# Kernel tuning notes

Measured on AMD Instinct MI355X. Metric: run time of the kernel, lower is better.

## Reference

```python
import jax, jax.numpy as jnp
import numpy as np

B, N, D, H = 4, 8192, 1024, 16
HD = D // H  # head dim 64
EPS = 1e-5


def setup_inputs() -> dict:
    key = jax.random.key(0)
    ks = jax.random.split(key, 12)
    s = 1.0 / np.sqrt(D)
    return {
        "query": jax.random.normal(ks[0], (B, N, D), jnp.float32),
        "Wq": jax.random.normal(ks[1], (D, D), jnp.float32) * s,
        "bq": jax.random.normal(ks[2], (D,), jnp.float32) * 0.01,
        "Wk": jax.random.normal(ks[3], (D, D), jnp.float32) * s,
        "bk": jax.random.normal(ks[4], (D,), jnp.float32) * 0.01,
        "Wv": jax.random.normal(ks[5], (D, D), jnp.float32) * s,
        "bv": jax.random.normal(ks[6], (D,), jnp.float32) * 0.01,
        "Wu": jax.random.normal(ks[7], (D, D), jnp.float32) * s,
        "bu": jax.random.normal(ks[8], (D,), jnp.float32) * 0.01,
        "Wo": jax.random.normal(ks[9], (D, D), jnp.float32) * s,
        "bo": jax.random.normal(ks[10], (D,), jnp.float32) * 0.01,
        "ln_w": jnp.ones((D,), jnp.float32),
        "ln_b": jnp.zeros((D,), jnp.float32),
    }


def _abs_clamp(t, min_mag=0.01, max_mag=100.0):
    return jnp.clip(jnp.abs(t), min_mag, max_mag) * jnp.sign(t)


def _heads(x):  # [b, n, h*d] -> [b, h, n, d]
    b, n, _ = x.shape
    return x.reshape(b, n, H, HD).transpose(0, 2, 1, 3)


def reference(query, Wq, bq, Wk, bk, Wv, bv, Wu, bu, Wo, bo, ln_w, ln_b):
    q = jax.nn.relu(_heads(query @ Wq + bq))  # [b,h,n,d]
    k = jax.nn.relu(_heads(query @ Wk + bk))
    v = _heads(query @ Wv + bv)
    u = query @ Wu + bu  # [b,n,D]
    # global linear-attention reduction: kv[b,h,d,e] = sum_n k v
    kv = jnp.einsum('bhnd,bhne->bhde', k, v)
    kv = _abs_clamp(kv)
    out = jnp.einsum('bhnd,bhde->bhne', q, kv)  # [b,h,n,d]
    out = out.transpose(0, 2, 1, 3).reshape(query.shape)  # [b,n,D]
    # LayerNorm over last dim
    mu = jnp.mean(out, axis=-1, keepdims=True)
    var = jnp.var(out, axis=-1, keepdims=True)
    out = (out - mu) * jax.lax.rsqrt(var + EPS) * ln_w + ln_b
    out = u * out
    return out @ Wo + bo
```

## Files before the change

### kernel.cpp

```cpp
#include <hip/hip_runtime.h>

#define M_TOT 32768

typedef float f32x4 __attribute__((ext_vector_type(4)));
typedef short s16x8 __attribute__((ext_vector_type(8)));

#define AS1(p) ((__attribute__((address_space(1))) void*)(p))
#define AS3(p) ((__attribute__((address_space(3))) void*)(p))

#define BARRIER() asm volatile("s_barrier" ::: "memory")
#define VMCNT8() asm volatile("s_waitcnt vmcnt(8)" ::: "memory")
#define VMCNT4() asm volatile("s_waitcnt vmcnt(4)" ::: "memory")
#define VMCNT0() asm volatile("s_waitcnt vmcnt(0)" ::: "memory")

__device__ __forceinline__ short f2bf(float f) {
    unsigned u = __builtin_bit_cast(unsigned, f);
    u += 0x7fffu + ((u >> 16) & 1u);
    return (short)(u >> 16);
}
__device__ __forceinline__ float bf2f(short s) {
    unsigned u = ((unsigned)(unsigned short)s) << 16;
    return __builtin_bit_cast(float, u);
}

__global__ void conv_x(const float* __restrict__ x, short* __restrict__ y) {
    const size_t nchunk = (size_t)M_TOT * 1024 / 8;
    const size_t stride = (size_t)gridDim.x * blockDim.x;
    for (size_t c = (size_t)blockIdx.x * blockDim.x + threadIdx.x; c < nchunk; c += stride) {
        const float4* src = (const float4*)(x + c * 8);
        float4 a = src[0], b = src[1];
        s16x8 r;
        r[0] = f2bf(a.x); r[1] = f2bf(a.y); r[2] = f2bf(a.z); r[3] = f2bf(a.w);
        r[4] = f2bf(b.x); r[5] = f2bf(b.y); r[6] = f2bf(b.z); r[7] = f2bf(b.w);
        *(s16x8*)(y + c * 8) = r;
    }
}

__global__ void conv_w(const float* __restrict__ Wq, const float* __restrict__ Wk,
                       const float* __restrict__ Wv, const float* __restrict__ Wu,
                       const float* __restrict__ Wo, short* __restrict__ Wcat) {
    const int c = blockIdx.x * 256 + threadIdx.x;
    const int np = c >> 8;
    const int k0 = (c & 255) << 2;
    const float* W = (np < 1024) ? Wq : (np < 2048) ? Wk : (np < 3072) ? Wv
                   : (np < 4096) ? Wu : Wo;
    const int n = np & 1023;
    short4 r;
    r.x = f2bf(W[(size_t)(k0 + 0) * 1024 + n]);
    r.y = f2bf(W[(size_t)(k0 + 1) * 1024 + n]);
    r.z = f2bf(W[(size_t)(k0 + 2) * 1024 + n]);
    r.w = f2bf(W[(size_t)(k0 + 3) * 1024 + n]);
    *(short4*)(Wcat + (size_t)np * 1024 + k0) = r;
}

__global__ void conv_bias(const float* __restrict__ bq, const float* __restrict__ bk,
                          const float* __restrict__ bv, const float* __restrict__ bu,
                          const float* __restrict__ bo, float* __restrict__ bcat) {
    const int i = blockIdx.x * 256 + threadIdx.x;
    const float* b = (i < 1024) ? bq : (i < 2048) ? bk : (i < 3072) ? bv
                   : (i < 4096) ? bu : bo;
    bcat[i] = b[i & 1023];
}

template <int MODE>
__global__ __launch_bounds__(512, 2) void gemm8(
        const short* __restrict__ A, const short* __restrict__ W,
        const float* __restrict__ bias,
        short* __restrict__ qb, short* __restrict__ ktb,
        short* __restrict__ vtb, short* __restrict__ ub,
        float* __restrict__ outb) {
    extern __shared__ char lds[];
    const int tid = threadIdx.x;
    const int wave = tid >> 6, lane = tid & 63;
    const int r16 = lane & 15;
    const int g2 = (((lane >> 4) ^ ((r16 >> 1) & 3)) << 4);
    const int srow = wave * 16 + (lane >> 2);
    const int scol = (((lane & 3) ^ ((lane >> 3) & 3)) << 4);
    const int moff = (wave >> 2) << 7;
    const int noff = (wave & 3) << 6;

    const int nwg = (MODE == 0) ? 2048 : 512;
    const int bid = blockIdx.x;
    const int swz = (bid & 7) * (nwg >> 3) + (bid >> 3);
    const int mblk = swz & 127, nblk = swz >> 7;
    const int row0 = mblk << 8, col0 = nblk << 8;

    const char* Agl = (const char*)A;
    const char* Wgl = (const char*)W;

#define STAGE(GB, R0, T, DST)                                                  \
    { _Pragma("unroll") for (int ld_ = 0; ld_ < 2; ++ld_) {                    \
        const char* g_ = (GB) + (size_t)((R0) + ld_ * 128 + srow) * 2048 +     \
                         (size_t)(T) * 64 + scol;                              \
        __builtin_amdgcn_global_load_lds(AS1(g_),                              \
            AS3((DST) + ld_ * 8192 + wave * 1024), 16, 0, 0); } }

#define RD(REG, RB) (*(const s16x8*)((REG) + ((RB) + r16) * 64 + g2))

    f32x4 acc[8][4] = {};
    s16x8 bfr[4];

    #pragma unroll
    for (int t = 0; t < 3; ++t) {
        char* dst = lds + (t & 3) * 32768;
        STAGE(Agl, row0, t, dst);
        STAGE(Wgl, col0, t, dst + 16384);
    }
    VMCNT8();
    BARRIER();

#define TILE(T, DOSTAGE, TRAIL)                                                \
    { char* Ar_ = lds + ((T) & 3) * 32768; char* Br_ = Ar_ + 16384;            \
      char* Sr_ = lds + (((T) + 3) & 3) * 32768;                               \
      s16x8 afr[4];                                                            \
      _Pragma("unroll") for (int n = 0; n < 4; ++n) bfr[n] = RD(Br_, noff + n * 16); \
      _Pragma("unroll") for (int m = 0; m < 4; ++m) afr[m] = RD(Ar_, moff + m * 16); \
      if (DOSTAGE) STAGE(Agl, row0, (T) + 3, Sr_);                             \
      BARRIER();                                                               \
      __builtin_amdgcn_s_setprio(1);                                           \
      _Pragma("unroll") for (int m = 0; m < 4; ++m)                            \
        _Pragma("unroll") for (int n = 0; n < 4; ++n)                          \
          acc[m][n] = __builtin_amdgcn_mfma_f32_16x16x32_bf16(afr[m], bfr[n], acc[m][n], 0, 0, 0); \
      __builtin_amdgcn_s_setprio(0);                                           \
      BARRIER();                                                               \
      _Pragma("unroll") for (int m = 0; m < 4; ++m) afr[m] = RD(Ar_, moff + 64 + m * 16); \
      if (DOSTAGE) STAGE(Wgl, col0, (T) + 3, Sr_ + 16384);                     \
      BARRIER();                                                               \
      __builtin_amdgcn_s_setprio(1);                                           \
      _Pragma("unroll") for (int m = 0; m < 4; ++m)                            \
        _Pragma("unroll") for (int n = 0; n < 4; ++n)                          \
          acc[m + 4][n] = __builtin_amdgcn_mfma_f32_16x16x32_bf16(afr[m], bfr[n], acc[m + 4][n], 0, 0, 0); \
      __builtin_amdgcn_s_setprio(0);                                           \
      TRAIL;                                                                   \
      BARRIER(); }

    #pragma unroll 1
    for (int t = 0; t < 29; ++t) TILE(t, true, VMCNT8());
    TILE(29, false, VMCNT4());
    TILE(30, false, VMCNT0());
    TILE(31, false, (void)0);

    const int rj = (lane >> 4) << 2;
    if (MODE == 1) {
        #pragma unroll
        for (int n = 0; n < 4; ++n) {
            const int gn = col0 + noff + n * 16 + r16;
            const float bv = bias[gn];
            #pragma unroll
            for (int m = 0; m < 8; ++m) {
                const int gm0 = row0 + moff + m * 16 + rj;
                #pragma unroll
                for (int j = 0; j < 4; ++j)
                    outb[(size_t)(gm0 + j) * 1024 + gn] = acc[m][n][j] + bv;
            }
        }
    } else {
        const int seg = col0 >> 10;
        if (seg == 0 || seg == 3) {
            short* dst = (seg == 0) ? qb : ub;
            const bool do_relu = (seg == 0);
            #pragma unroll
            for (int n = 0; n < 4; ++n) {
                const int gn = col0 + noff + n * 16 + r16;
                const int f = gn & 1023;
                const float bv = bias[gn];
                #pragma unroll
                for (int m = 0; m < 8; ++m) {
                    const int gm0 = row0 + moff + m * 16 + rj;
                    #pragma unroll
                    for (int j = 0; j < 4; ++j) {
                        float val = acc[m][n][j] + bv;
                        if (do_relu) val = fmaxf(val, 0.0f);
                        dst[(size_t)(gm0 + j) * 1024 + f] = f2bf(val);
                    }
                }
            }
        } else {
            short* dst = (seg == 1) ? ktb : vtb;
            const bool do_relu = (seg == 1);
            #pragma unroll
            for (int n = 0; n < 4; ++n) {
                const int gn = col0 + noff + n * 16 + r16;
                const int hd = gn & 1023;
                const float bv = bias[gn];
                #pragma unroll
                for (int m = 0; m < 8; ++m) {
                    const int gm0 = row0 + moff + m * 16 + rj;
                    const int b = gm0 >> 13;
                    const int ntok = gm0 & 8191;
                    float v0 = acc[m][n][0] + bv, v1 = acc[m][n][1] + bv;
                    float v2 = acc[m][n][2] + bv, v3 = acc[m][n][3] + bv;
                    if (do_relu) {
                        v0 = fmaxf(v0, 0.0f); v1 = fmaxf(v1, 0.0f);
                        v2 = fmaxf(v2, 0.0f); v3 = fmaxf(v3, 0.0f);
                    }
                    short4 pk;
                    pk.x = f2bf(v0); pk.y = f2bf(v1); pk.z = f2bf(v2); pk.w = f2bf(v3);
                    *(short4*)(dst + ((size_t)(b * 1024 + hd)) * 8192 + ntok) = pk;
                }
            }
        }
    }
#undef TILE
#undef RD
#undef STAGE
}

__global__ __launch_bounds__(64) void kv_partial(const short* __restrict__ ktb,
                                                 const short* __restrict__ vtb,
                                                 float* __restrict__ kvp) {
    const int slice = blockIdx.x;
    const int bh = blockIdx.y;
    const int lane = threadIdx.x;
    const int r16 = lane & 15;
    const short* kb = ktb + (size_t)bh * 64 * 8192;
    const short* vb = vtb + (size_t)bh * 64 * 8192;
    const int n0 = slice << 8;
    f32x4 acc[4][4] = {};
    for (int s = 0; s < 8; ++s) {
        const int nk = n0 + (s << 5) + ((lane >> 4) << 3);
        s16x8 af[4], bf[4];
        #pragma unroll
        for (int m = 0; m < 4; ++m) af[m] = *(const s16x8*)(kb + (size_t)(m * 16 + r16) * 8192 + nk);
        #pragma unroll
        for (int n = 0; n < 4; ++n) bf[n] = *(const s16x8*)(vb + (size_t)(n * 16 + r16) * 8192 + nk);
        #pragma unroll
        for (int m = 0; m < 4; ++m)
            #pragma unroll
            for (int n = 0; n < 4; ++n)
                acc[m][n] = __builtin_amdgcn_mfma_f32_16x16x32_bf16(af[m], bf[n], acc[m][n], 0, 0, 0);
    }
    float* dst = kvp + ((size_t)slice * 64 + bh) * 4096;
    const int rj = (lane >> 4) << 2;
    #pragma unroll
    for (int m = 0; m < 4; ++m)
        #pragma unroll
        for (int n = 0; n < 4; ++n)
            #pragma unroll
            for (int j = 0; j < 4; ++j)
                dst[(size_t)(m * 16 + rj + j) * 64 + n * 16 + r16] = acc[m][n][j];
}

__global__ void kv_reduce(const float* __restrict__ kvp, short* __restrict__ kvt) {
    const int bh = blockIdx.x;
    for (int i = threadIdx.x; i < 4096; i += 256) {
        float s = 0.0f;
        #pragma unroll 8
        for (int sl = 0; sl < 32; ++sl)
            s += kvp[((size_t)sl * 64 + bh) * 4096 + i];
        float a = fabsf(s);
        float cmag = fminf(fmaxf(a, 0.01f), 100.0f);
        float r = (s > 0.0f) ? cmag : ((s < 0.0f) ? -cmag : 0.0f);
        const int d = i >> 6, e = i & 63;
        kvt[(size_t)bh * 4096 + e * 64 + d] = f2bf(r);
    }
}

__global__ __launch_bounds__(256) void qkv_out(const short* __restrict__ qb,
                                               const short* __restrict__ kvt,
                                               float* __restrict__ ob) {
    const int bh = blockIdx.y;
    const int b = bh >> 4, h = bh & 15;
    const int tid = threadIdx.x;
    const int wave = tid >> 6, lane = tid & 63;
    const int r16 = lane & 15;
    const size_t mbase = (size_t)b * 8192 + ((size_t)blockIdx.x << 8) + (wave << 6);
    const short* kvb = kvt + (size_t)bh * 4096;
    f32x4 acc[4][4] = {};
    #pragma unroll
    for (int s = 0; s < 2; ++s) {
        const int kq2 = (s << 5) + ((lane >> 4) << 3);
        s16x8 af[4], bf[4];
        #pragma unroll
        for (int m = 0; m < 4; ++m)
            af[m] = *(const s16x8*)(qb + (mbase + m * 16 + r16) * 1024 + h * 64 + kq2);
        #pragma unroll
        for (int n = 0; n < 4; ++n)
            bf[n] = *(const s16x8*)(kvb + (n * 16 + r16) * 64 + kq2);
        #pragma unroll
        for (int m = 0; m < 4; ++m)
            #pragma unroll
            for (int n = 0; n < 4; ++n)
                acc[m][n] = __builtin_amdgcn_mfma_f32_16x16x32_bf16(af[m], bf[n], acc[m][n], 0, 0, 0);
    }
    const int rj = (lane >> 4) << 2;
    #pragma unroll
    for (int m = 0; m < 4; ++m)
        #pragma unroll
        for (int n = 0; n < 4; ++n)
            #pragma unroll
            for (int j = 0; j < 4; ++j)
                ob[(mbase + m * 16 + rj + j) * 1024 + h * 64 + n * 16 + r16] = acc[m][n][j];
}

__global__ __launch_bounds__(256) void ln_mul(const float* __restrict__ ob,
                                              const short* __restrict__ ub,
                                              const float* __restrict__ lnw,
                                              const float* __restrict__ lnb,
                                              short* __restrict__ yb) {
    const int row = blockIdx.x;
    const int tid = threadIdx.x;
    const float4 v = ((const float4*)(ob + (size_t)row * 1024))[tid];
    float s = v.x + v.y + v.z + v.w;
    float sq = v.x * v.x + v.y * v.y + v.z * v.z + v.w * v.w;
    #pragma unroll
    for (int off = 32; off > 0; off >>= 1) {
        s += __shfl_down(s, off);
        sq += __shfl_down(sq, off);
    }
    __shared__ float ls[4], lq[4];
    const int wave = tid >> 6, lane = tid & 63;
    if (lane == 0) { ls[wave] = s; lq[wave] = sq; }
    __syncthreads();
    const float S = ls[0] + ls[1] + ls[2] + ls[3];
    const float SQ = lq[0] + lq[1] + lq[2] + lq[3];
    const float mu = S * (1.0f / 1024.0f);
    const float var = SQ * (1.0f / 1024.0f) - mu * mu;
    const float rs = rsqrtf(var + 1e-5f);
    const short4 uu = ((const short4*)(ub + (size_t)row * 1024))[tid];
    const float4 w = ((const float4*)lnw)[tid];
    const float4 bb = ((const float4*)lnb)[tid];
    short4 o;
    o.x = f2bf(bf2f(uu.x) * ((v.x - mu) * rs * w.x + bb.x));
    o.y = f2bf(bf2f(uu.y) * ((v.y - mu) * rs * w.y + bb.y));
    o.z = f2bf(bf2f(uu.z) * ((v.z - mu) * rs * w.z + bb.z));
    o.w = f2bf(bf2f(uu.w) * ((v.w - mu) * rs * w.w + bb.w));
    ((short4*)(yb + (size_t)row * 1024))[tid] = o;
}

extern "C" void kernel_launch(void* const* d_in, const int* in_sizes, int n_in,
                              void* d_out, int out_size, void* d_ws, size_t ws_size,
                              hipStream_t stream) {
    (void)in_sizes; (void)n_in; (void)out_size;
    const float* query = (const float*)d_in[0];
    const float* Wq = (const float*)d_in[1];
    const float* bq = (const float*)d_in[2];
    const float* Wk = (const float*)d_in[3];
    const float* bk = (const float*)d_in[4];
    const float* Wv = (const float*)d_in[5];
    const float* bv = (const float*)d_in[6];
    const float* Wu = (const float*)d_in[7];
    const float* bu = (const float*)d_in[8];
    const float* Wo = (const float*)d_in[9];
    const float* bo = (const float*)d_in[10];
    const float* lnw = (const float*)d_in[11];
    const float* lnb = (const float*)d_in[12];
    float* out = (float*)d_out;
    char* ws = (char*)d_ws;
    if (ws_size < 380129280u) return;

    short* Xb   = (short*)(ws);
    short* Wcat = (short*)(ws + 67108864);
    float* bcat = (float*)(ws + 77594624);
    short* qb   = (short*)(ws + 77615104);
    short* ktb  = (short*)(ws + 144723968);
    short* vtb  = (short*)(ws + 211832832);
    short* ub   = (short*)(ws + 278941696);
    float* kvp  = (float*)(ws + 346050560);
    short* kvt  = (short*)(ws + 379604992);
    float* ob   = (float*)(ws + 144723968);
    short* yb   = Xb;

    hipFuncSetAttribute(reinterpret_cast<const void*>(&gemm8<0>),
                        hipFuncAttributeMaxDynamicSharedMemorySize, 131072);
    hipFuncSetAttribute(reinterpret_cast<const void*>(&gemm8<1>),
                        hipFuncAttributeMaxDynamicSharedMemorySize, 131072);

    conv_x<<<2048, 256, 0, stream>>>(query, Xb);
    conv_w<<<5120, 256, 0, stream>>>(Wq, Wk, Wv, Wu, Wo, Wcat);
    conv_bias<<<20, 256, 0, stream>>>(bq, bk, bv, bu, bo, bcat);
    gemm8<0><<<2048, 512, 131072, stream>>>(Xb, Wcat, bcat, qb, ktb, vtb, ub, nullptr);
    kv_partial<<<dim3(32, 64), 64, 0, stream>>>(ktb, vtb, kvp);
    kv_reduce<<<64, 256, 0, stream>>>(kvp, kvt);
    qkv_out<<<dim3(32, 64), 256, 0, stream>>>(qb, kvt, ob);
    ln_mul<<<32768, 256, 0, stream>>>(ob, ub, lnw, lnb, yb);
    gemm8<1><<<512, 512, 131072, stream>>>(yb, Wcat + (size_t)4096 * 1024, bcat + 4096,
                                           nullptr, nullptr, nullptr, nullptr, out);
}
```

Baseline: 657.5 us.

## Restructure GEMM pipeline to double-buffered K=64 tiles with interleaved staging

Changes the bf16 GEMM main loop from a 4-deep ring of K=32 tiles to a 2-deep double buffer of K=64 tiles. Global-to-LDS staging is split into four chunks interleaved between four MFMA phases. The block-to-tile mapping switches to m-major ordering via division by the number of n-blocks, and the LDS XOR swizzle is widened to 8 chunks per 128-byte row. The aim is fewer barriers per K element and better L2 reuse of the weight tiles. The cost is a shallower prefetch depth, which may expose more global memory latency.

Measured after the change: 600.5 us. 8.7% less time.

```diff
diff --git a/kernel.cpp b/kernel.cpp
--- a/kernel.cpp
+++ b/kernel.cpp
@@ -9,8 +9,8 @@
 #define AS3(p) ((__attribute__((address_space(3))) void*)(p))
 
 #define BARRIER() asm volatile("s_barrier" ::: "memory")
-#define VMCNT8() asm volatile("s_waitcnt vmcnt(8)" ::: "memory")
 #define VMCNT4() asm volatile("s_waitcnt vmcnt(4)" ::: "memory")
+#define VMCNT2() asm volatile("s_waitcnt vmcnt(2)" ::: "memory")
 #define VMCNT0() asm volatile("s_waitcnt vmcnt(0)" ::: "memory")
 
 __device__ __forceinline__ short f2bf(float f) {
@@ -72,73 +72,85 @@
     extern __shared__ char lds[];
     const int tid = threadIdx.x;
     const int wave = tid >> 6, lane = tid & 63;
-    const int r16 = lane & 15;
-    const int g2 = (((lane >> 4) ^ ((r16 >> 1) & 3)) << 4);
-    const int srow = wave * 16 + (lane >> 2);
-    const int scol = (((lane & 3) ^ ((lane >> 3) & 3)) << 4);
+    const int r16 = lane & 15, g = lane >> 4;
     const int moff = (wave >> 2) << 7;
     const int noff = (wave & 3) << 6;
 
     const int nwg = (MODE == 0) ? 2048 : 512;
+    const int NB = (MODE == 0) ? 16 : 4;
     const int bid = blockIdx.x;
     const int swz = (bid & 7) * (nwg >> 3) + (bid >> 3);
-    const int mblk = swz & 127, nblk = swz >> 7;
+    const int mblk = swz / NB, nblk = swz % NB;
     const int row0 = mblk << 8, col0 = nblk << 8;
 
-    const char* Agl = (const char*)A;
-    const char* Wgl = (const char*)W;
-
-#define STAGE(GB, R0, T, DST)                                                  \
-    { _Pragma("unroll") for (int ld_ = 0; ld_ < 2; ++ld_) {                    \
-        const char* g_ = (GB) + (size_t)((R0) + ld_ * 128 + srow) * 2048 +     \
-                         (size_t)(T) * 64 + scol;                              \
-        __builtin_amdgcn_global_load_lds(AS1(g_),                              \
-            AS3((DST) + ld_ * 8192 + wave * 1024), 16, 0, 0); } }
-
-#define RD(REG, RB) (*(const s16x8*)((REG) + ((RB) + r16) * 64 + g2))
+    const int rswz = r16 & 7;
+    const int ck0 = (g ^ rswz) << 4;
+    const int ck1 = ((4 + g) ^ rswz) << 4;
+    const int rowbA = (moff + r16) << 7;
+    const int rowbB = (noff + r16) << 7;
+
+    const char* baseA = (const char*)A + (size_t)(row0 + wave * 8 + (lane >> 3)) * 2048
+                        + (((lane & 7) ^ ((lane >> 3) & 7)) << 4);
+    const char* baseB = (const char*)W + (size_t)(col0 + wave * 8 + (lane >> 3)) * 2048
+                        + (((lane & 7) ^ ((lane >> 3) & 7)) << 4);
+
+#define STG(BASE, J, T, DST)                                                   \
+    __builtin_amdgcn_global_load_lds(                                          \
+        AS1((BASE) + (size_t)(J) * 131072 + (size_t)(T) * 128),                \
+        AS3((DST) + (J) * 8192 + wave * 1024), 16, 0, 0)
+
+#define RDA(V, M, BUFA) {                                                      \
+    (V)[0] = *(const s16x8*)((BUFA) + rowbA + (M) * 2048 + ck0);               \
+    (V)[1] = *(const s16x8*)((BUFA) + rowbA + (M) * 2048 + ck1); }
+
+#define RDB(V, N, BUFB) {                                                      \
+    (V)[0] = *(const s16x8*)((BUFB) + rowbB + (N) * 2048 + ck0);               \
+    (V)[1] = *(const s16x8*)((BUFB) + rowbB + (N) * 2048 + ck1); }
+
+#define MF16(P)                                                                \
+    _Pragma("unroll") for (int n = 0; n < 4; ++n) {                            \
+        acc[2*(P)][n]   = __builtin_amdgcn_mfma_f32_16x16x32_bf16(afr[0][0], bfr[n][0], acc[2*(P)][n], 0, 0, 0);   \
+        acc[2*(P)+1][n] = __builtin_amdgcn_mfma_f32_16x16x32_bf16(afr[1][0], bfr[n][0], acc[2*(P)+1][n], 0, 0, 0); \
+        acc[2*(P)][n]   = __builtin_amdgcn_mfma_f32_16x16x32_bf16(afr[0][1], bfr[n][1], acc[2*(P)][n], 0, 0, 0);   \
+        acc[2*(P)+1][n] = __builtin_amdgcn_mfma_f32_16x16x32_bf16(afr[1][1], bfr[n][1], acc[2*(P)+1][n], 0, 0, 0); \
+    }
+
+#define TILE(T, DOSTAGE, TR2, TR4) {                                           \
+    char* bA_ = lds + ((T) & 1) * 65536; char* bB_ = bA_ + 32768;              \
+    char* sA_ = lds + (((T) + 1) & 1) * 65536; char* sB_ = sA_ + 32768;        \
+    s16x8 afr[2][2];                                                           \
+    if (DOSTAGE) { STG(baseB, 0, (T) + 1, sB_); STG(baseB, 1, (T) + 1, sB_); } \
+    _Pragma("unroll") for (int n = 0; n < 4; ++n) RDB(bfr[n], n, bB_);         \
+    RDA(afr[0], 0, bA_); RDA(afr[1], 1, bA_);                                  \
+    BARRIER(); __builtin_amdgcn_s_setprio(1); MF16(0);                         \
+    __builtin_amdgcn_s_setprio(0); BARRIER();                                  \
+    if (DOSTAGE) { STG(baseB, 2, (T) + 1, sB_); STG(baseB, 3, (T) + 1, sB_); } \
+    RDA(afr[0], 2, bA_); RDA(afr[1], 3, bA_);                                  \
+    BARRIER(); __builtin_amdgcn_s_setprio(1); MF16(1);                         \
+    __builtin_amdgcn_s_setprio(0); TR2; BARRIER();                             \
+    if (DOSTAGE) { STG(baseA, 0, (T) + 1, sA_); STG(baseA, 2, (T) + 1, sA_); } \
+    RDA(afr[0], 4, bA_); RDA(afr[1], 5, bA_);                                  \
+    BARRIER(); __builtin_amdgcn_s_setprio(1); MF16(2);                         \
+    __builtin_amdgcn_s_setprio(0); BARRIER();                                  \
+    if (DOSTAGE) { STG(baseA, 1, (T) + 1, sA_); STG(baseA, 3, (T) + 1, sA_); } \
+    RDA(afr[0], 6, bA_); RDA(afr[1], 7, bA_);                                  \
+    BARRIER(); __builtin_amdgcn_s_setprio(1); MF16(3);                         \
+    __builtin_amdgcn_s_setprio(0); TR4; BARRIER();                             \
+}
 
     f32x4 acc[8][4] = {};
-    s16x8 bfr[4];
-
-    #pragma unroll
-    for (int t = 0; t < 3; ++t) {
-        char* dst = lds + (t & 3) * 32768;
-        STAGE(Agl, row0, t, dst);
-        STAGE(Wgl, col0, t, dst + 16384);
-    }
-    VMCNT8();
+    s16x8 bfr[4][2];
+
+    STG(baseB, 0, 0, lds + 32768); STG(baseB, 1, 0, lds + 32768);
+    STG(baseB, 2, 0, lds + 32768); STG(baseB, 3, 0, lds + 32768);
+    STG(baseA, 0, 0, lds);         STG(baseA, 2, 0, lds);
+    STG(baseA, 1, 0, lds);         STG(baseA, 3, 0, lds);
+    VMCNT2();
     BARRIER();
 
-#define TILE(T, DOSTAGE, TRAIL)                                                \
-    { char* Ar_ = lds + ((T) & 3) * 32768; char* Br_ = Ar_ + 16384;            \
-      char* Sr_ = lds + (((T) + 3) & 3) * 32768;                               \
-      s16x8 afr[4];                                                            \
-      _Pragma("unroll") for (int n = 0; n < 4; ++n) bfr[n] = RD(Br_, noff + n * 16); \
-      _Pragma("unroll") for (int m = 0; m < 4; ++m) afr[m] = RD(Ar_, moff + m * 16); \
-      if (DOSTAGE) STAGE(Agl, row0, (T) + 3, Sr_);                             \
-      BARRIER();                                                               \
-      __builtin_amdgcn_s_setprio(1);                                           \
-      _Pragma("unroll") for (int m = 0; m < 4; ++m)                            \
-        _Pragma("unroll") for (int n = 0; n < 4; ++n)                          \
-          acc[m][n] = __builtin_amdgcn_mfma_f32_16x16x32_bf16(afr[m], bfr[n], acc[m][n], 0, 0, 0); \
-      __builtin_amdgcn_s_setprio(0);                                           \
-      BARRIER();                                                               \
-      _Pragma("unroll") for (int m = 0; m < 4; ++m) afr[m] = RD(Ar_, moff + 64 + m * 16); \
-      if (DOSTAGE) STAGE(Wgl, col0, (T) + 3, Sr_ + 16384);                     \
-      BARRIER();                                                               \
-      __builtin_amdgcn_s_setprio(1);                                           \
-      _Pragma("unroll") for (int m = 0; m < 4; ++m)                            \
-        _Pragma("unroll") for (int n = 0; n < 4; ++n)                          \
-          acc[m + 4][n] = __builtin_amdgcn_mfma_f32_16x16x32_bf16(afr[m], bfr[n], acc[m + 4][n], 0, 0, 0); \
-      __builtin_amdgcn_s_setprio(0);                                           \
-      TRAIL;                                                                   \
-      BARRIER(); }
-
     #pragma unroll 1
-    for (int t = 0; t < 29; ++t) TILE(t, true, VMCNT8());
-    TILE(29, false, VMCNT4());
-    TILE(30, false, VMCNT0());
-    TILE(31, false, (void)0);
+    for (int t = 0; t < 15; ++t) TILE(t, true, VMCNT4(), VMCNT2());
+    TILE(15, false, VMCNT0(), (void)0);
 
     const int rj = (lane >> 4) << 2;
     if (MODE == 1) {
@@ -202,8 +214,10 @@
         }
     }
 #undef TILE
-#undef RD
-#undef STAGE
+#undef MF16
+#undef RDB
+#undef RDA
+#undef STG
 }
 
 __global__ __launch_bounds__(64) void kv_partial(const short* __restrict__ ktb,
```
